# Kernel optimization log

Measured on AMD Instinct MI355X. Metric: run time of the kernel, lower is better.

The kernel has to match this reference:

```python
import jax, jax.numpy as jnp
import numpy as np

B = 256
N_SNP = 100000
BITS = 4          # snp_onehot_bits
BLOCK = 20        # SNPs per block
N_BLOCKS = N_SNP // BLOCK            # 5000 output blocks
IN_DIM = N_SNP * BITS                # 400000
DIMS = [1024, 256]
OUT_DIM = 1
LN_EPS = 1e-5


def _make_indices():
    # blocks_gt[i] = [20*i, ..., 20*i+19]; replicate get_param4sparse
    blocks = np.arange(N_SNP, dtype=np.int64).reshape(N_BLOCKS, BLOCK)
    idx0 = (blocks[:, :, None] * BITS + np.arange(BITS)).reshape(-1)   # input bit index, [nnz]
    idx1 = np.repeat(np.arange(N_BLOCKS, dtype=np.int64), BLOCK * BITS)  # output block index, [nnz]
    return jnp.asarray(idx0, jnp.int32), jnp.asarray(idx1, jnp.int32)


def setup_inputs() -> dict:
    key = jax.random.key(0)
    ks = jax.random.split(key, 9)
    idx0, idx1 = _make_indices()
    x = jax.random.uniform(ks[0], (B, IN_DIM), dtype=jnp.float32)
    sparse_values = jax.random.normal(ks[1], (idx0.shape[0],), dtype=jnp.float32)
    ln_gamma = jnp.ones((N_BLOCKS,), jnp.float32)
    ln_beta = jnp.zeros((N_BLOCKS,), jnp.float32)
    s1 = 1.0 / np.sqrt(N_BLOCKS)
    W1 = jax.random.uniform(ks[2], (DIMS[0], N_BLOCKS), jnp.float32, -s1, s1)
    b1 = jax.random.uniform(ks[3], (DIMS[0],), jnp.float32, -s1, s1)
    s2 = 1.0 / np.sqrt(DIMS[0])
    W2 = jax.random.uniform(ks[4], (DIMS[1], DIMS[0]), jnp.float32, -s2, s2)
    b2 = jax.random.uniform(ks[5], (DIMS[1],), jnp.float32, -s2, s2)
    s3 = 1.0 / np.sqrt(DIMS[1])
    W3 = jax.random.uniform(ks[6], (OUT_DIM, DIMS[1]), jnp.float32, -s3, s3)
    b3 = jax.random.uniform(ks[7], (OUT_DIM,), jnp.float32, -s3, s3)
    return {"x": x, "sparse_values": sparse_values, "ln_gamma": ln_gamma,
            "ln_beta": ln_beta, "W1": W1, "b1": b1, "W2": W2, "b2": b2,
            "W3": W3, "b3": b3, "idx0": idx0, "idx1": idx1}


def reference(x, sparse_values, ln_gamma, ln_beta, W1, b1, W2, b2, W3, b3, idx0, idx1):
    # SparseLinear: out[b, j] = sum_{k: idx1[k]==j} sparse_values[k] * x[b, idx0[k]]
    gathered = x[:, idx0] * sparse_values[None, :]                       # [B, nnz]
    gblocks = jax.ops.segment_sum(gathered.T, idx1, num_segments=N_BLOCKS).T  # [B, n_blocks]
    # LayerNorm over block dim
    mu = jnp.mean(gblocks, axis=-1, keepdims=True)
    var = jnp.mean(jnp.square(gblocks - mu), axis=-1, keepdims=True)
    h = (gblocks - mu) * jax.lax.rsqrt(var + LN_EPS) * ln_gamma + ln_beta
    # Dense head (note: no activation after first Linear, faithful to source)
    h = h @ W1.T + b1
    h = h @ W2.T + b2
    h = jax.nn.sigmoid(h)
    return h @ W3.T + b3                                                 # [B, OUT_DIM]
```

## Files before the change

### kernel.cpp

```cpp
#include <hip/hip_runtime.h>
#include <math.h>

#define BATCH   256
#define NBLK    5000
#define NBLKP   5024
#define IN_DIM  400000
#define D1      1024
#define D2      256
#define K1P     5120
#define NSPLIT  8
#define KSPLIT  (K1P / NSPLIT)

typedef __attribute__((ext_vector_type(8))) short short8_t;
typedef __attribute__((ext_vector_type(4))) float f32x4;

static __device__ __forceinline__ unsigned short f2bf(float f) {
    union { float f; unsigned int u; } v; v.f = f;
    unsigned int u = v.u;
    return (unsigned short)((u + 0x7FFFu + ((u >> 16) & 1u)) >> 16);
}

__global__ __launch_bounds__(256) void k_sparse(const float* __restrict__ x,
                                                const float* __restrict__ sv,
                                                float* __restrict__ g) {
    const int b   = blockIdx.y;
    const int tid = threadIdx.x;
    const int jj  = tid >> 2;
    const int s   = tid & 3;
    const int j   = blockIdx.x * 64 + jj;
    if (j >= NBLK) {
        if (j < NBLKP && s == 0) g[(size_t)b * NBLKP + j] = 0.0f;
        return;
    }
    const float4* xr = reinterpret_cast<const float4*>(x + (size_t)b * IN_DIM + (size_t)j * 80);
    const float4* sr = reinterpret_cast<const float4*>(sv + (size_t)j * 80);
    float acc = 0.0f;
#pragma unroll
    for (int r = 0; r < 5; ++r) {
        float4 xv = xr[r * 4 + s];
        float4 sg = sr[r * 4 + s];
        acc += xv.x * sg.x + xv.y * sg.y + xv.z * sg.z + xv.w * sg.w;
    }
    acc += __shfl_xor(acc, 1);
    acc += __shfl_xor(acc, 2);
    if (s == 0) g[(size_t)b * NBLKP + j] = acc;
}

__global__ __launch_bounds__(256) void k_ln(const float* __restrict__ g,
                                            const float* __restrict__ gamma,
                                            const float* __restrict__ beta,
                                            unsigned short* __restrict__ A) {
    const int b   = blockIdx.x;
    const int tid = threadIdx.x;
    const float* row = g + (size_t)b * NBLKP;
    float v[20];
    float s = 0.0f, ss = 0.0f;
#pragma unroll
    for (int i = 0; i < 20; ++i) {
        const int j = tid + i * 256;
        const float xv = (j < NBLK) ? row[j] : 0.0f;
        v[i] = xv; s += xv; ss += xv * xv;
    }
#pragma unroll
    for (int o = 32; o > 0; o >>= 1) {
        s  += __shfl_xor(s, o);
        ss += __shfl_xor(ss, o);
    }
    __shared__ float ls[4], lss[4];
    const int wid = tid >> 6;
    if ((tid & 63) == 0) { ls[wid] = s; lss[wid] = ss; }
    __syncthreads();
    s  = ls[0] + ls[1] + ls[2] + ls[3];
    ss = lss[0] + lss[1] + lss[2] + lss[3];
    const float mu  = s / (float)NBLK;
    const float var = ss / (float)NBLK - mu * mu;
    const float rs  = rsqrtf(var + 1e-5f);
    unsigned short* dst = A + (size_t)b * K1P;
#pragma unroll
    for (int i = 0; i < 20; ++i) {
        const int j = tid + i * 256;
        const float val = (j < NBLK) ? ((v[i] - mu) * rs * gamma[j] + beta[j]) : 0.0f;
        dst[j] = f2bf(val);
    }
}

__global__ __launch_bounds__(256) void k_conv(const float* __restrict__ W1,
                                              unsigned short* __restrict__ W1b,
                                              const float* __restrict__ W2,
                                              unsigned short* __restrict__ W2b) {
    const int blk = blockIdx.x;
    if (blk < D1) {
        const float* src = W1 + (size_t)blk * NBLK;
        unsigned short* dst = W1b + (size_t)blk * K1P;
        for (int c4 = threadIdx.x; c4 < K1P / 4; c4 += 256) {
            const int c = c4 * 4;
            ushort4 o;
            if (c < NBLK) {
                float4 v = *reinterpret_cast<const float4*>(src + c);
                o = { f2bf(v.x), f2bf(v.y), f2bf(v.z), f2bf(v.w) };
            } else {
                o = ushort4{0, 0, 0, 0};
            }
            *reinterpret_cast<ushort4*>(dst + c) = o;
        }
    } else {
        const int idx = ((blk - D1) * 256 + threadIdx.x) * 4;
        float4 v = *reinterpret_cast<const float4*>(W2 + idx);
        ushort4 o = { f2bf(v.x), f2bf(v.y), f2bf(v.z), f2bf(v.w) };
        *reinterpret_cast<ushort4*>(W2b + idx) = o;
    }
}

template <int LDK, int LDC, bool SIG>
__global__ __launch_bounds__(256) void k_mfma_gemm(const unsigned short* __restrict__ A,
                                                   const unsigned short* __restrict__ W,
                                                   const float* __restrict__ bias,
                                                   float* __restrict__ C,
                                                   int ksteps, int Mtotal) {
    const int m0 = blockIdx.y * 64;
    const int n0 = blockIdx.x * 64;
    const int z  = blockIdx.z;
    const int kbase = z * ksteps * 64;
    float* Cz = C + (size_t)z * (size_t)Mtotal * LDC;

    __shared__ unsigned short As[64][72];
    __shared__ unsigned short Ws[64][72];

    const int tid  = threadIdx.x;
    const int wave = tid >> 6;
    const int lane = tid & 63;
    const int wr   = (wave >> 1) * 32;
    const int wc   = (wave & 1) * 32;
    const int lr   = lane & 15;
    const int lk   = (lane >> 4) * 8;
    const int srow = tid >> 3;
    const int scol = (tid & 7) * 8;

    const unsigned short* Ap = A + (size_t)(m0 + srow) * LDK + kbase + scol;
    const unsigned short* Wp = W + (size_t)(n0 + srow) * LDK + kbase + scol;

    short8_t pa0 = *reinterpret_cast<const short8_t*>(Ap);
    short8_t pa1 = *reinterpret_cast<const short8_t*>(Ap + (size_t)32 * LDK);
    short8_t pw0 = *reinterpret_cast<const short8_t*>(Wp);
    short8_t pw1 = *reinterpret_cast<const short8_t*>(Wp + (size_t)32 * LDK);

    f32x4 acc[2][2] = {};

    for (int t = 0; t < ksteps; ++t) {
        __syncthreads();
        *reinterpret_cast<short8_t*>(&As[srow][scol])      = pa0;
        *reinterpret_cast<short8_t*>(&As[srow + 32][scol]) = pa1;
        *reinterpret_cast<short8_t*>(&Ws[srow][scol])      = pw0;
        *reinterpret_cast<short8_t*>(&Ws[srow + 32][scol]) = pw1;
        __syncthreads();
        if (t + 1 < ksteps) {
            const unsigned short* An = Ap + (size_t)(t + 1) * 64;
            const unsigned short* Wn = Wp + (size_t)(t + 1) * 64;
            pa0 = *reinterpret_cast<const short8_t*>(An);
            pa1 = *reinterpret_cast<const short8_t*>(An + (size_t)32 * LDK);
            pw0 = *reinterpret_cast<const short8_t*>(Wn);
            pw1 = *reinterpret_cast<const short8_t*>(Wn + (size_t)32 * LDK);
        }
#pragma unroll
        for (int kk = 0; kk < 64; kk += 32) {
            short8_t a0 = *reinterpret_cast<const short8_t*>(&As[wr + lr][kk + lk]);
            short8_t a1 = *reinterpret_cast<const short8_t*>(&As[wr + 16 + lr][kk + lk]);
            short8_t b0 = *reinterpret_cast<const short8_t*>(&Ws[wc + lr][kk + lk]);
            short8_t b1 = *reinterpret_cast<const short8_t*>(&Ws[wc + 16 + lr][kk + lk]);
            acc[0][0] = __builtin_amdgcn_mfma_f32_16x16x32_bf16(a0, b0, acc[0][0], 0, 0, 0);
            acc[0][1] = __builtin_amdgcn_mfma_f32_16x16x32_bf16(a0, b1, acc[0][1], 0, 0, 0);
            acc[1][0] = __builtin_amdgcn_mfma_f32_16x16x32_bf16(a1, b0, acc[1][0], 0, 0, 0);
            acc[1][1] = __builtin_amdgcn_mfma_f32_16x16x32_bf16(a1, b1, acc[1][1], 0, 0, 0);
        }
    }

    const int rbase = (lane >> 4) * 4;
#pragma unroll
    for (int i = 0; i < 2; ++i)
#pragma unroll
        for (int j = 0; j < 2; ++j) {
            const int col = n0 + wc + j * 16 + lr;
            const float bv = SIG ? bias[col] : 0.0f;
#pragma unroll
            for (int r = 0; r < 4; ++r) {
                const int row = m0 + wr + i * 16 + rbase + r;
                float v = acc[i][j][r] + bv;
                if (SIG) v = 1.0f / (1.0f + __expf(-v));
                Cz[(size_t)row * LDC + col] = v;
            }
        }
}

__global__ __launch_bounds__(256) void k_fuse(const float* __restrict__ p,
                                              const float* __restrict__ b1,
                                              unsigned short* __restrict__ A2) {
    const int idx = (blockIdx.x * 256 + threadIdx.x) * 4;
    const int col = idx & (D1 - 1);
    const size_t S = (size_t)BATCH * D1;
    float4 bb = *reinterpret_cast<const float4*>(b1 + col);
    float sx = bb.x, sy = bb.y, sz = bb.z, sw = bb.w;
#pragma unroll
    for (int q = 0; q < NSPLIT; ++q) {
        float4 v = *reinterpret_cast<const float4*>(p + q * S + idx);
        sx += v.x; sy += v.y; sz += v.z; sw += v.w;
    }
    ushort4 o = { f2bf(sx), f2bf(sy), f2bf(sz), f2bf(sw) };
    *reinterpret_cast<ushort4*>(A2 + idx) = o;
}

__global__ __launch_bounds__(64) void k_out(const float* __restrict__ h2,
                                            const float* __restrict__ W3,
                                            const float* __restrict__ b3,
                                            float* __restrict__ out) {
    const int b = blockIdx.x;
    const int l = threadIdx.x;
    float acc = 0.0f;
#pragma unroll
    for (int o = 0; o < D2; o += 64) acc += h2[(size_t)b * D2 + o + l] * W3[o + l];
#pragma unroll
    for (int o = 32; o > 0; o >>= 1) acc += __shfl_xor(acc, o);
    if (l == 0) out[b] = acc + b3[0];
}

extern "C" void kernel_launch(void* const* d_in, const int* in_sizes, int n_in,
                              void* d_out, int out_size, void* d_ws, size_t ws_size,
                              hipStream_t stream) {
    const float* x     = (const float*)d_in[0];
    const float* sv    = (const float*)d_in[1];
    const float* gamma = (const float*)d_in[2];
    const float* beta  = (const float*)d_in[3];
    const float* W1    = (const float*)d_in[4];
    const float* b1    = (const float*)d_in[5];
    const float* W2    = (const float*)d_in[6];
    const float* b2    = (const float*)d_in[7];
    const float* W3    = (const float*)d_in[8];
    const float* b3    = (const float*)d_in[9];
    float* out = (float*)d_out;

    char* ws = (char*)d_ws;
    size_t off = 0;
    auto alloc = [&](size_t bytes) { char* p = ws + off; off = (off + bytes + 255) & ~(size_t)255; return p; };
    float*          g     = (float*)         alloc((size_t)BATCH * NBLKP * 4);
    unsigned short* Ab    = (unsigned short*)alloc((size_t)BATCH * K1P * 2);
    unsigned short* W1b   = (unsigned short*)alloc((size_t)D1 * K1P * 2);
    float*          out1p = (float*)         alloc((size_t)NSPLIT * BATCH * D1 * 4);
    unsigned short* A2b   = (unsigned short*)alloc((size_t)BATCH * D1 * 2);
    unsigned short* W2b   = (unsigned short*)alloc((size_t)D2 * D1 * 2);
    float*          h2    = (float*)         alloc((size_t)BATCH * D2 * 4);

    k_conv<<<dim3(D1 + D2 * D1 / 1024), 256, 0, stream>>>(W1, W1b, W2, W2b);
    k_sparse<<<dim3((NBLKP + 63) / 64, BATCH), 256, 0, stream>>>(x, sv, g);
    k_ln<<<dim3(BATCH), 256, 0, stream>>>(g, gamma, beta, Ab);
    k_mfma_gemm<K1P, D1, false>
        <<<dim3(D1 / 64, BATCH / 64, NSPLIT), 256, 0, stream>>>(Ab, W1b, nullptr, out1p, KSPLIT / 64, BATCH);
    k_fuse<<<dim3(BATCH * D1 / (256 * 4)), 256, 0, stream>>>(out1p, b1, A2b);
    k_mfma_gemm<D1, D2, true>
        <<<dim3(D2 / 64, BATCH / 64, 1), 256, 0, stream>>>(A2b, W2b, b2, h2, D1 / 64, BATCH);
    k_out<<<dim3(BATCH), 64, 0, stream>>>(h2, W3, b3, out);
}
```

Before: 132.7 us.

## Fuse weight conversion with sparse stage and fuse GEMM2, sigmoid and output head

Merges the W1/W2 bf16 conversion and the sparse block reduction into one launch, with the grid split between the two jobs by block index. Replaces the second GEMM, its sigmoid epilogue and the final dot-product kernel with a single tail kernel. That kernel computes a 32-row by 256-column tile per block and reduces sigmoid(h)·W3 through shuffles and shared memory. This removes two kernel launches and the h2 round trip through global memory. The cost is that the tail runs on only 8 blocks, each streaming all of W2, which leaves most of the GPU idle during that stage.

```diff
diff --git a/kernel.cpp b/kernel.cpp
--- a/kernel.cpp
+++ b/kernel.cpp
@@ -11,6 +11,9 @@
 #define NSPLIT  8
 #define KSPLIT  (K1P / NSPLIT)
 
+#define CONV_BLKS   (D1 + D2 * D1 / 1024)
+#define SPARSE_BLKS ((NBLKP + 63) / 64 * BATCH)
+
 typedef __attribute__((ext_vector_type(8))) short short8_t;
 typedef __attribute__((ext_vector_type(4))) float f32x4;
 
@@ -20,18 +23,45 @@
     return (unsigned short)((u + 0x7FFFu + ((u >> 16) & 1u)) >> 16);
 }
 
-__global__ __launch_bounds__(256) void k_sparse(const float* __restrict__ x,
+__global__ __launch_bounds__(256) void k_stage1(const float* __restrict__ x,
                                                 const float* __restrict__ sv,
-                                                float* __restrict__ g) {
-    const int b   = blockIdx.y;
+                                                float* __restrict__ g,
+                                                const float* __restrict__ W1,
+                                                unsigned short* __restrict__ W1b,
+                                                const float* __restrict__ W2,
+                                                unsigned short* __restrict__ W2b) {
+    const int id  = blockIdx.x;
     const int tid = threadIdx.x;
+    if (id < CONV_BLKS) {
+        if (id < D1) {
+            const float* src = W1 + (size_t)id * NBLK;
+            unsigned short* dst = W1b + (size_t)id * K1P;
+            for (int c4 = tid; c4 < K1P / 4; c4 += 256) {
+                const int c = c4 * 4;
+                ushort4 o;
+                if (c < NBLK) {
+                    float4 v = *reinterpret_cast<const float4*>(src + c);
+                    o = { f2bf(v.x), f2bf(v.y), f2bf(v.z), f2bf(v.w) };
+                } else {
+                    o = ushort4{0, 0, 0, 0};
+                }
+                *reinterpret_cast<ushort4*>(dst + c) = o;
+            }
+        } else {
+            const int idx = ((id - D1) * 256 + tid) * 4;
+            float4 v = *reinterpret_cast<const float4*>(W2 + idx);
+            ushort4 o = { f2bf(v.x), f2bf(v.y), f2bf(v.z), f2bf(v.w) };
+            *reinterpret_cast<ushort4*>(W2b + idx) = o;
+        }
+        return;
+    }
+    const int rem = id - CONV_BLKS;
+    const int b   = rem / ((NBLKP + 63) / 64);
+    const int bx  = rem % ((NBLKP + 63) / 64);
     const int jj  = tid >> 2;
     const int s   = tid & 3;
-    const int j   = blockIdx.x * 64 + jj;
-    if (j >= NBLK) {
-        if (j < NBLKP && s == 0) g[(size_t)b * NBLKP + j] = 0.0f;
-        return;
-    }
+    const int j   = bx * 64 + jj;
+    if (j >= NBLK) return;
     const float4* xr = reinterpret_cast<const float4*>(x + (size_t)b * IN_DIM + (size_t)j * 80);
     const float4* sr = reinterpret_cast<const float4*>(sv + (size_t)j * 80);
     float acc = 0.0f;
@@ -84,44 +114,15 @@
     }
 }
 
-__global__ __launch_bounds__(256) void k_conv(const float* __restrict__ W1,
-                                              unsigned short* __restrict__ W1b,
-                                              const float* __restrict__ W2,
-                                              unsigned short* __restrict__ W2b) {
-    const int blk = blockIdx.x;
-    if (blk < D1) {
-        const float* src = W1 + (size_t)blk * NBLK;
-        unsigned short* dst = W1b + (size_t)blk * K1P;
-        for (int c4 = threadIdx.x; c4 < K1P / 4; c4 += 256) {
-            const int c = c4 * 4;
-            ushort4 o;
-            if (c < NBLK) {
-                float4 v = *reinterpret_cast<const float4*>(src + c);
-                o = { f2bf(v.x), f2bf(v.y), f2bf(v.z), f2bf(v.w) };
-            } else {
-                o = ushort4{0, 0, 0, 0};
-            }
-            *reinterpret_cast<ushort4*>(dst + c) = o;
-        }
-    } else {
-        const int idx = ((blk - D1) * 256 + threadIdx.x) * 4;
-        float4 v = *reinterpret_cast<const float4*>(W2 + idx);
-        ushort4 o = { f2bf(v.x), f2bf(v.y), f2bf(v.z), f2bf(v.w) };
-        *reinterpret_cast<ushort4*>(W2b + idx) = o;
-    }
-}
-
-template <int LDK, int LDC, bool SIG>
-__global__ __launch_bounds__(256) void k_mfma_gemm(const unsigned short* __restrict__ A,
-                                                   const unsigned short* __restrict__ W,
-                                                   const float* __restrict__ bias,
-                                                   float* __restrict__ C,
-                                                   int ksteps, int Mtotal) {
+__global__ __launch_bounds__(256) void k_mfma_gemm1(const unsigned short* __restrict__ A,
+                                                    const unsigned short* __restrict__ W,
+                                                    float* __restrict__ C,
+                                                    int ksteps) {
     const int m0 = blockIdx.y * 64;
     const int n0 = blockIdx.x * 64;
     const int z  = blockIdx.z;
     const int kbase = z * ksteps * 64;
-    float* Cz = C + (size_t)z * (size_t)Mtotal * LDC;
+    float* Cz = C + (size_t)z * (size_t)BATCH * D1;
 
     __shared__ unsigned short As[64][72];
     __shared__ unsigned short Ws[64][72];
@@ -136,13 +137,13 @@
     const int srow = tid >> 3;
     const int scol = (tid & 7) * 8;
 
-    const unsigned short* Ap = A + (size_t)(m0 + srow) * LDK + kbase + scol;
-    const unsigned short* Wp = W + (size_t)(n0 + srow) * LDK + kbase + scol;
+    const unsigned short* Ap = A + (size_t)(m0 + srow) * K1P + kbase + scol;
+    const unsigned short* Wp = W + (size_t)(n0 + srow) * K1P + kbase + scol;
 
     short8_t pa0 = *reinterpret_cast<const short8_t*>(Ap);
-    short8_t pa1 = *reinterpret_cast<const short8_t*>(Ap + (size_t)32 * LDK);
+    short8_t pa1 = *reinterpret_cast<const short8_t*>(Ap + (size_t)32 * K1P);
     short8_t pw0 = *reinterpret_cast<const short8_t*>(Wp);
-    short8_t pw1 = *reinterpret_cast<const short8_t*>(Wp + (size_t)32 * LDK);
+    short8_t pw1 = *reinterpret_cast<const short8_t*>(Wp + (size_t)32 * K1P);
 
     f32x4 acc[2][2] = {};
 
@@ -157,9 +158,9 @@
             const unsigned short* An = Ap + (size_t)(t + 1) * 64;
             const unsigned short* Wn = Wp + (size_t)(t + 1) * 64;
             pa0 = *reinterpret_cast<const short8_t*>(An);
-            pa1 = *reinterpret_cast<const short8_t*>(An + (size_t)32 * LDK);
+            pa1 = *reinterpret_cast<const short8_t*>(An + (size_t)32 * K1P);
             pw0 = *reinterpret_cast<const short8_t*>(Wn);
-            pw1 = *reinterpret_cast<const short8_t*>(Wn + (size_t)32 * LDK);
+            pw1 = *reinterpret_cast<const short8_t*>(Wn + (size_t)32 * K1P);
         }
 #pragma unroll
         for (int kk = 0; kk < 64; kk += 32) {
@@ -180,13 +181,10 @@
 #pragma unroll
         for (int j = 0; j < 2; ++j) {
             const int col = n0 + wc + j * 16 + lr;
-            const float bv = SIG ? bias[col] : 0.0f;
 #pragma unroll
             for (int r = 0; r < 4; ++r) {
                 const int row = m0 + wr + i * 16 + rbase + r;
-                float v = acc[i][j][r] + bv;
-                if (SIG) v = 1.0f / (1.0f + __expf(-v));
-                Cz[(size_t)row * LDC + col] = v;
+                Cz[(size_t)row * D1 + col] = acc[i][j][r];
             }
         }
 }
@@ -208,18 +206,94 @@
     *reinterpret_cast<ushort4*>(A2 + idx) = o;
 }
 
-__global__ __launch_bounds__(64) void k_out(const float* __restrict__ h2,
-                                            const float* __restrict__ W3,
-                                            const float* __restrict__ b3,
-                                            float* __restrict__ out) {
-    const int b = blockIdx.x;
-    const int l = threadIdx.x;
-    float acc = 0.0f;
-#pragma unroll
-    for (int o = 0; o < D2; o += 64) acc += h2[(size_t)b * D2 + o + l] * W3[o + l];
-#pragma unroll
-    for (int o = 32; o > 0; o >>= 1) acc += __shfl_xor(acc, o);
-    if (l == 0) out[b] = acc + b3[0];
+__global__ __launch_bounds__(256) void k_tail(const unsigned short* __restrict__ A2,
+                                              const unsigned short* __restrict__ W2b,
+                                              const float* __restrict__ b2,
+                                              const float* __restrict__ W3,
+                                              const float* __restrict__ b3,
+                                              float* __restrict__ out) {
+    const int m0 = blockIdx.x * 32;
+    __shared__ unsigned short As[32][72];
+    __shared__ unsigned short Ws[256][72];
+    __shared__ float red[4][32];
+
+    const int tid  = threadIdx.x;
+    const int wave = tid >> 6;
+    const int lane = tid & 63;
+    const int wc   = wave * 64;
+    const int lr   = lane & 15;
+    const int lk   = (lane >> 4) * 8;
+    const int srow = tid >> 3;
+    const int scol = (tid & 7) * 8;
+
+    const unsigned short* Ap = A2 + (size_t)(m0 + srow) * D1 + scol;
+    const unsigned short* Wp = W2b + (size_t)srow * D1 + scol;
+
+    short8_t pa = *reinterpret_cast<const short8_t*>(Ap);
+    short8_t pw[8];
+#pragma unroll
+    for (int it = 0; it < 8; ++it)
+        pw[it] = *reinterpret_cast<const short8_t*>(Wp + (size_t)it * 32 * D1);
+
+    f32x4 acc[2][4] = {};
+
+    for (int t = 0; t < 16; ++t) {
+        __syncthreads();
+        *reinterpret_cast<short8_t*>(&As[srow][scol]) = pa;
+#pragma unroll
+        for (int it = 0; it < 8; ++it)
+            *reinterpret_cast<short8_t*>(&Ws[srow + it * 32][scol]) = pw[it];
+        __syncthreads();
+        if (t + 1 < 16) {
+            const int ko = (t + 1) * 64;
+            pa = *reinterpret_cast<const short8_t*>(Ap + ko);
+#pragma unroll
+            for (int it = 0; it < 8; ++it)
+                pw[it] = *reinterpret_cast<const short8_t*>(Wp + (size_t)it * 32 * D1 + ko);
+        }
+#pragma unroll
+        for (int kk = 0; kk < 64; kk += 32) {
+            short8_t a0 = *reinterpret_cast<const short8_t*>(&As[lr][kk + lk]);
+            short8_t a1 = *reinterpret_cast<const short8_t*>(&As[16 + lr][kk + lk]);
+#pragma unroll
+            for (int j = 0; j < 4; ++j) {
+                short8_t bj = *reinterpret_cast<const short8_t*>(&Ws[wc + j * 16 + lr][kk + lk]);
+                acc[0][j] = __builtin_amdgcn_mfma_f32_16x16x32_bf16(a0, bj, acc[0][j], 0, 0, 0);
+                acc[1][j] = __builtin_amdgcn_mfma_f32_16x16x32_bf16(a1, bj, acc[1][j], 0, 0, 0);
+            }
+        }
+    }
+
+    float b2c[4], w3c[4];
+#pragma unroll
+    for (int j = 0; j < 4; ++j) {
+        const int col = wc + j * 16 + lr;
+        b2c[j] = b2[col];
+        w3c[j] = W3[col];
+    }
+    const int rbase = (lane >> 4) * 4;
+#pragma unroll
+    for (int i = 0; i < 2; ++i) {
+#pragma unroll
+        for (int r = 0; r < 4; ++r) {
+            float pv = 0.0f;
+#pragma unroll
+            for (int j = 0; j < 4; ++j) {
+                const float h = acc[i][j][r] + b2c[j];
+                pv += w3c[j] / (1.0f + __expf(-h));
+            }
+            pv += __shfl_xor(pv, 1);
+            pv += __shfl_xor(pv, 2);
+            pv += __shfl_xor(pv, 4);
+            pv += __shfl_xor(pv, 8);
+            if (lr == 0) red[wave][i * 16 + rbase + r] = pv;
+        }
+    }
+    __syncthreads();
+    if (tid < 32) {
+        const float s = red[0][tid] + red[1][tid] + red[2][tid] + red[3][tid];
+        out[m0 + tid] = s + b3[0];
+    }
 }
 
 extern "C" void kernel_launch(void* const* d_in, const int* in_sizes, int n_in,
@@ -246,15 +320,10 @@
     float*          out1p = (float*)         alloc((size_t)NSPLIT * BATCH * D1 * 4);
     unsigned short* A2b   = (unsigned short*)alloc((size_t)BATCH * D1 * 2);
     unsigned short* W2b   = (unsigned short*)alloc((size_t)D2 * D1 * 2);
-    float*          h2    = (float*)         alloc((size_t)BATCH * D2 * 4);
-
-    k_conv<<<dim3(D1 + D2 * D1 / 1024), 256, 0, stream>>>(W1, W1b, W2, W2b);
-    k_sparse<<<dim3((NBLKP + 63) / 64, BATCH), 256, 0, stream>>>(x, sv, g);
+
+    k_stage1<<<dim3(CONV_BLKS + SPARSE_BLKS), 256, 0, stream>>>(x, sv, g, W1, W1b, W2, W2b);
     k_ln<<<dim3(BATCH), 256, 0, stream>>>(g, gamma, beta, Ab);
-    k_mfma_gemm<K1P, D1, false>
-        <<<dim3(D1 / 64, BATCH / 64, NSPLIT), 256, 0, stream>>>(Ab, W1b, nullptr, out1p, KSPLIT / 64, BATCH);
+    k_mfma_gemm1<<<dim3(D1 / 64, BATCH / 64, NSPLIT), 256, 0, stream>>>(Ab, W1b, out1p, KSPLIT / 64);
     k_fuse<<<dim3(BATCH * D1 / (256 * 4)), 256, 0, stream>>>(out1p, b1, A2b);
-    k_mfma_gemm<D1, D2, true>
-        <<<dim3(D2 / 64, BATCH / 64, 1), 256, 0, stream>>>(A2b, W2b, b2, h2, D1 / 64, BATCH);
-    k_out<<<dim3(BATCH), 64, 0, stream>>>(h2, W3, b3, out);
-}
+    k_tail<<<dim3(BATCH / 32), 256, 0, stream>>>(A2b, W2b, b2, W3, b3, out);
+}
```

Result: slower. 136.9 us (+3.2%).
